# Performance work log

Measured on AMD Instinct MI355X. Metric: run time of the kernel, lower is better.

Reference implementation:

```python
import jax, jax.numpy as jnp
import numpy as np

N_NODES = 100000
N_EDGES = 3200000
F_IN, F_HID, F_OUT = 1433, 8, 7
K = 2  # kernel_size, dim=1, degree-1 B-spline -> basis (1-u, u)
LEAKY_SLOPE = 0.2


def att_spline_conv(x, edge_index, pseudo, w, root, att, bias, n_nodes):
    """Attention SplineConv layer (dim=1, kernel_size=2, linear B-spline).

    w:    [K, in, out] spline kernel weights
    root: [in, out]    root/self weight
    att:  [2*out]      attention vector (src-message part || dst part)
    """
    src, dst = edge_index[0], edge_index[1]
    u = pseudo[:, 0]                                   # [E], in [0,1]
    basis = jnp.stack([1.0 - u, u], axis=1)            # [E, K]
    # transform at node level first (cheap), then gather per edge
    xw = jnp.einsum('ni,kio->nko', x, w)               # [N, K, out]
    m = jnp.einsum('ek,eko->eo', basis, xw[src])       # [E, out] spline message
    h = x @ root                                       # [N, out] root transform
    out_dim = w.shape[-1]
    # GAT-style attention: leaky_relu(a_src . m_e + a_dst . h_dst)
    score = m @ att[:out_dim] + (h @ att[out_dim:])[dst]   # [E]
    score = jax.nn.leaky_relu(score, LEAKY_SLOPE)
    smax = jax.ops.segment_max(score, dst, num_segments=n_nodes)
    e = jnp.exp(score - smax[dst])
    denom = jax.ops.segment_sum(e, dst, num_segments=n_nodes)
    alpha = e / (denom[dst] + 1e-16)                   # segment softmax over dst
    agg = jax.ops.segment_sum(alpha[:, None] * m, dst, num_segments=n_nodes)
    return agg + h + bias


def setup_inputs() -> dict:
    key = jax.random.key(0)
    ks = jax.random.split(key, 12)
    x = jax.random.normal(ks[0], (N_NODES, F_IN), dtype=jnp.float32)
    edge_index = jax.random.randint(ks[1], (2, N_EDGES), 0, N_NODES, dtype=jnp.int64)
    pseudo = jax.random.uniform(ks[2], (N_EDGES, 1), dtype=jnp.float32)
    s1 = 1.0 / np.sqrt(F_IN)
    s2 = 1.0 / np.sqrt(F_HID)
    return {
        'x': x,
        'edge_index': edge_index,
        'pseudo': pseudo,
        'w1': jax.random.normal(ks[3], (K, F_IN, F_HID), dtype=jnp.float32) * s1,
        'root1': jax.random.normal(ks[4], (F_IN, F_HID), dtype=jnp.float32) * s1,
        'att1': jax.random.normal(ks[5], (2 * F_HID,), dtype=jnp.float32) * s2,
        'bias1': jnp.zeros((F_HID,), dtype=jnp.float32),
        'w2': jax.random.normal(ks[6], (K, F_HID, F_OUT), dtype=jnp.float32) * s2,
        'root2': jax.random.normal(ks[7], (F_HID, F_OUT), dtype=jnp.float32) * s2,
        'att2': jax.random.normal(ks[8], (2 * F_OUT,), dtype=jnp.float32) * s2,
        'bias2': jnp.zeros((F_OUT,), dtype=jnp.float32),
    }


def reference(x, edge_index, pseudo, w1, root1, att1, bias1, w2, root2, att2, bias2):
    # eval mode: F.dropout with training=False is identity
    n = x.shape[0]
    h = jax.nn.elu(att_spline_conv(x, edge_index, pseudo, w1, root1, att1, bias1, n))
    h = att_spline_conv(h, edge_index, pseudo, w2, root2, att2, bias2, n)
    return jax.nn.log_softmax(h, axis=1)
```

## Files before the change

### kernel.cpp

```cpp
#include <hip/hip_runtime.h>
#include <math.h>

#define TPB 256
#define F_IN 1433
#define KPAD 1440
#define NT 45
#define NFULL 44
#define ROWS 128

typedef __attribute__((ext_vector_type(8))) short bf16x8;
typedef __attribute__((ext_vector_type(4))) float f32x4;

static __device__ __forceinline__ short f2bf(float f) {
    unsigned u = __float_as_uint(f);
    unsigned r = (u + 0x7FFFu + ((u >> 16) & 1u)) >> 16;
    return (short)r;
}

__global__ __launch_bounds__(256) void prep_kernel(
    const float* __restrict__ w1, const float* __restrict__ root1,
    short* __restrict__ WT, int* __restrict__ cnt, int N)
{
    int i = blockIdx.x * 256 + threadIdx.x;
    if (i < N) cnt[i] = 0;
    if (i < 32 * KPAD) {
        int col = i / KPAD, k = i - col * KPAD;
        float v = 0.f;
        if (k < F_IN) {
            if (col < 8)       v = w1[(size_t)k * 8 + col];
            else if (col < 16) v = w1[(size_t)(F_IN + k) * 8 + (col - 8)];
            else if (col < 24) v = root1[(size_t)k * 8 + (col - 16)];
        }
        WT[i] = f2bf(v);
    }
}

__global__ __launch_bounds__(256) void node1_hist_kernel(
    const float* __restrict__ x,
    const short* __restrict__ WT,
    const float* __restrict__ att1,
    float* __restrict__ XW1,
    float* __restrict__ H1,
    float2* __restrict__ SC1,
    float* __restrict__ HA1,
    const int* __restrict__ ei,
    int* __restrict__ cnt,
    int N, int E, int NB1)
{
    __shared__ float xb[4][32][32];

    const int tid = threadIdx.x;
    const int bid = blockIdx.x;

    if (bid >= NB1) {
        int e = (bid - NB1) * TPB + tid;
        if (e < E) atomicAdd(&cnt[ei[(size_t)E + e]], 1);
        return;
    }

    const int wv   = tid >> 6;
    const int lane = tid & 63;
    const int rowbase = bid * ROWS;

    const int srow   = lane & 7;
    const int schunk = lane >> 3;
    const int pchunk = schunk ^ srow;
    const float* gsrc[4];
#pragma unroll
    for (int g = 0; g < 4; ++g) {
        int r = rowbase + wv * 32 + g * 8 + srow;
        if (r >= N) r = N - 1;
        gsrc[g] = x + (size_t)r * F_IN + schunk * 4;
    }

    const int r0 = lane & 15, r1 = r0 + 16;
    const int klane = (lane >> 4) * 8;
    const int c0 = klane >> 2;
    const int p0 = c0 ^ (r0 & 7);
    const int p1 = (c0 + 1) ^ (r0 & 7);
    const short* wt0 = WT + (size_t)(lane & 15) * KPAD + klane;
    const short* wt1 = wt0 + 16 * KPAD;

    f32x4 acc[2][2];
#pragma unroll
    for (int i = 0; i < 2; ++i)
#pragma unroll
        for (int j = 0; j < 2; ++j)
#pragma unroll
            for (int r = 0; r < 4; ++r) acc[i][j][r] = 0.f;

    {
        float4 V[4];
#pragma unroll
        for (int g = 0; g < 4; ++g) V[g] = *reinterpret_cast<const float4*>(gsrc[g]);
#pragma unroll
        for (int g = 0; g < 4; ++g)
            *reinterpret_cast<float4*>(&xb[wv][g * 8 + srow][pchunk * 4]) = V[g];
    }

    for (int t = 0; t < NFULL; ++t) {
        float4 Vn[4];
        const bool more = (t + 1 < NFULL);
        if (more) {
#pragma unroll
            for (int g = 0; g < 4; ++g)
                Vn[g] = *reinterpret_cast<const float4*>(gsrc[g] + (t + 1) * 32);
        }
        bf16x8 b0 = *reinterpret_cast<const bf16x8*>(wt0 + t * 32);
        bf16x8 b1 = *reinterpret_cast<const bf16x8*>(wt1 + t * 32);
        float4 fa0 = *reinterpret_cast<const float4*>(&xb[wv][r0][p0 * 4]);
        float4 fb0 = *reinterpret_cast<const float4*>(&xb[wv][r0][p1 * 4]);
        float4 fa1 = *reinterpret_cast<const float4*>(&xb[wv][r1][p0 * 4]);
        float4 fb1 = *reinterpret_cast<const float4*>(&xb[wv][r1][p1 * 4]);
        bf16x8 pa0, pa1;
        pa0[0] = f2bf(fa0.x); pa0[1] = f2bf(fa0.y); pa0[2] = f2bf(fa0.z); pa0[3] = f2bf(fa0.w);
        pa0[4] = f2bf(fb0.x); pa0[5] = f2bf(fb0.y); pa0[6] = f2bf(fb0.z); pa0[7] = f2bf(fb0.w);
        pa1[0] = f2bf(fa1.x); pa1[1] = f2bf(fa1.y); pa1[2] = f2bf(fa1.z); pa1[3] = f2bf(fa1.w);
        pa1[4] = f2bf(fb1.x); pa1[5] = f2bf(fb1.y); pa1[6] = f2bf(fb1.z); pa1[7] = f2bf(fb1.w);
        acc[0][0] = __builtin_amdgcn_mfma_f32_16x16x32_bf16(pa0, b0, acc[0][0], 0, 0, 0);
        acc[0][1] = __builtin_amdgcn_mfma_f32_16x16x32_bf16(pa0, b1, acc[0][1], 0, 0, 0);
        acc[1][0] = __builtin_amdgcn_mfma_f32_16x16x32_bf16(pa1, b0, acc[1][0], 0, 0, 0);
        acc[1][1] = __builtin_amdgcn_mfma_f32_16x16x32_bf16(pa1, b1, acc[1][1], 0, 0, 0);
        if (more) {
#pragma unroll
            for (int g = 0; g < 4; ++g)
                *reinterpret_cast<float4*>(&xb[wv][g * 8 + srow][pchunk * 4]) = Vn[g];
        }
    }

    {
        int rr0 = rowbase + wv * 32 + r0; if (rr0 >= N) rr0 = N - 1;
        int rr1 = rowbase + wv * 32 + r1; if (rr1 >= N) rr1 = N - 1;
        const float* xr0 = x + (size_t)rr0 * F_IN;
        const float* xr1 = x + (size_t)rr1 * F_IN;
        const int kf = NFULL * 32 + klane;
        bf16x8 pa0, pa1;
#pragma unroll
        for (int q = 0; q < 8; ++q) {
            float v0 = (kf + q < F_IN) ? xr0[kf + q] : 0.f;
            float v1 = (kf + q < F_IN) ? xr1[kf + q] : 0.f;
            pa0[q] = f2bf(v0);
            pa1[q] = f2bf(v1);
        }
        bf16x8 b0 = *reinterpret_cast<const bf16x8*>(wt0 + NFULL * 32);
        bf16x8 b1 = *reinterpret_cast<const bf16x8*>(wt1 + NFULL * 32);
        acc[0][0] = __builtin_amdgcn_mfma_f32_16x16x32_bf16(pa0, b0, acc[0][0], 0, 0, 0);
        acc[0][1] = __builtin_amdgcn_mfma_f32_16x16x32_bf16(pa0, b1, acc[0][1], 0, 0, 0);
        acc[1][0] = __builtin_amdgcn_mfma_f32_16x16x32_bf16(pa1, b0, acc[1][0], 0, 0, 0);
        acc[1][1] = __builtin_amdgcn_mfma_f32_16x16x32_bf16(pa1, b1, acc[1][1], 0, 0, 0);
    }

    __syncthreads();

    float* dump = reinterpret_cast<float*>(xb);
#pragma unroll
    for (int rt = 0; rt < 2; ++rt)
#pragma unroll
        for (int ot = 0; ot < 2; ++ot) {
            int col = ot * 16 + (lane & 15);
            if (col < 24) {
#pragma unroll
                for (int r = 0; r < 4; ++r) {
                    int row = wv * 32 + rt * 16 + (lane >> 4) * 4 + r;
                    dump[row * 25 + col] = acc[rt][ot][r];
                }
            }
        }
    __syncthreads();

    if (tid < ROWS) {
        int n = rowbase + tid;
        if (n < N) {
            float sum[24];
#pragma unroll
            for (int j = 0; j < 24; ++j) sum[j] = dump[tid * 25 + j];
            float s0 = 0.f, s1 = 0.f, ha = 0.f;
#pragma unroll
            for (int j = 0; j < 8; ++j) {
                s0 += sum[j] * att1[j];
                s1 += sum[8 + j] * att1[j];
                ha += sum[16 + j] * att1[8 + j];
            }
            float4* xwout = reinterpret_cast<float4*>(XW1 + (size_t)n * 16);
            xwout[0] = make_float4(sum[0], sum[1], sum[2], sum[3]);
            xwout[1] = make_float4(sum[4], sum[5], sum[6], sum[7]);
            xwout[2] = make_float4(sum[8], sum[9], sum[10], sum[11]);
            xwout[3] = make_float4(sum[12], sum[13], sum[14], sum[15]);
            float4* hout = reinterpret_cast<float4*>(H1 + (size_t)n * 8);
            hout[0] = make_float4(sum[16], sum[17], sum[18], sum[19]);
            hout[1] = make_float4(sum[20], sum[21], sum[22], sum[23]);
            SC1[n] = make_float2(s0, s1);
            HA1[n] = ha;
        }
    }
}

__global__ __launch_bounds__(256) void scanA_kernel(
    const int* __restrict__ cnt, int* __restrict__ rowptr, int* __restrict__ bsums, int N)
{
    __shared__ int lds[256];
    int t = threadIdx.x;
    int base = blockIdx.x * 1024 + t * 4;
    int c[4];
#pragma unroll
    for (int j = 0; j < 4; ++j) c[j] = (base + j < N) ? cnt[base + j] : 0;
    int tsum = c[0] + c[1] + c[2] + c[3];
    lds[t] = tsum;
    __syncthreads();
    for (int off = 1; off < 256; off <<= 1) {
        int v = (t >= off) ? lds[t - off] : 0;
        __syncthreads();
        lds[t] += v;
        __syncthreads();
    }
    int run = lds[t] - tsum;
#pragma unroll
    for (int j = 0; j < 4; ++j) {
        if (base + j < N) rowptr[base + j] = run;
        run += c[j];
    }
    if (t == 255) bsums[blockIdx.x] = lds[255];
}

__global__ __launch_bounds__(128) void scanB_kernel(int* __restrict__ bsums, int nb)
{
    __shared__ int lds[128];
    int t = threadIdx.x;
    int v = (t < nb) ? bsums[t] : 0;
    lds[t] = v;
    __syncthreads();
    for (int off = 1; off < 128; off <<= 1) {
        int w = (t >= off) ? lds[t - off] : 0;
        __syncthreads();
        lds[t] += w;
        __syncthreads();
    }
    if (t < nb) bsums[t] = lds[t] - v;
}

__global__ __launch_bounds__(256) void scanC_kernel(
    int* __restrict__ rowptr, int* __restrict__ cnt, const int* __restrict__ bsums, int N, int E)
{
    int i = blockIdx.x * TPB + threadIdx.x;
    if (i < N) {
        int v = rowptr[i] + bsums[i >> 10];
        rowptr[i] = v;
        cnt[i] = v;
    }
    if (i == 0) rowptr[N] = E;
}

__global__ __launch_bounds__(256) void scatter_kernel(
    const int* __restrict__ ei, const float* __restrict__ pseudo,
    int* __restrict__ cursor, int2* __restrict__ recs, int E)
{
    int e = blockIdx.x * TPB + threadIdx.x;
    if (e >= E) return;
    int s = ei[e];
    int d = ei[(size_t)E + e];
    float u = pseudo[e];
    int pos = atomicAdd(&cursor[d], 1);
    recs[pos] = make_int2(s, __float_as_int(u));
}

__global__ __launch_bounds__(256) void gather1_kernel(
    const int* __restrict__ rowptr, const int2* __restrict__ recs,
    const float4* __restrict__ XW1v,
    const float2* __restrict__ SC1, const float* __restrict__ HA1,
    const float* __restrict__ H1, const float* __restrict__ bias1,
    const float* __restrict__ w2, const float* __restrict__ root2, const float* __restrict__ att2,
    float* __restrict__ XW2, float* __restrict__ H2, float2* __restrict__ SC2, float* __restrict__ HA2,
    int N)
{
    int tid = blockIdx.x * TPB + threadIdx.x;
    int n = tid >> 4;
    int lane = tid & 15;
    if (n >= N) return;
    int start = rowptr[n], end = rowptr[n + 1];
    float ha = HA1[n];
    float den = 0.f;
    float num[8];
#pragma unroll
    for (int j = 0; j < 8; ++j) num[j] = 0.f;

    for (int i = start + lane; i < end; i += 16) {
        int2 r = recs[i];
        int s = r.x;
        float u = __int_as_float(r.y);
        float um = 1.f - u;
        float2 sc = SC1[s];
        float raw = um * sc.x + u * sc.y + ha;
        float score = (raw > 0.f) ? raw : 0.2f * raw;
        float w = expf(score);
        const float4* xw = XW1v + (size_t)s * 4;
        float4 p0 = xw[0], p1 = xw[1], q0 = xw[2], q1 = xw[3];
        num[0] = fmaf(w, um * p0.x + u * q0.x, num[0]);
        num[1] = fmaf(w, um * p0.y + u * q0.y, num[1]);
        num[2] = fmaf(w, um * p0.z + u * q0.z, num[2]);
        num[3] = fmaf(w, um * p0.w + u * q0.w, num[3]);
        num[4] = fmaf(w, um * p1.x + u * q1.x, num[4]);
        num[5] = fmaf(w, um * p1.y + u * q1.y, num[5]);
        num[6] = fmaf(w, um * p1.z + u * q1.z, num[6]);
        num[7] = fmaf(w, um * p1.w + u * q1.w, num[7]);
        den += w;
    }
#pragma unroll
    for (int off = 1; off < 16; off <<= 1) {
#pragma unroll
        for (int j = 0; j < 8; ++j) num[j] += __shfl_xor(num[j], off);
        den += __shfl_xor(den, off);
    }
    if (lane != 0) return;

    float inv = 1.f / (den + 1e-16f);
    float hp[8];
#pragma unroll
    for (int j = 0; j < 8; ++j) {
        float o = num[j] * inv + H1[(size_t)n * 8 + j] + bias1[j];
        hp[j] = (o > 0.f) ? o : expm1f(o);
    }
    float a[7], b[7], h[7];
#pragma unroll
    for (int j2 = 0; j2 < 7; ++j2) { a[j2] = 0.f; b[j2] = 0.f; h[j2] = 0.f; }
#pragma unroll
    for (int j = 0; j < 8; ++j) {
#pragma unroll
        for (int j2 = 0; j2 < 7; ++j2) {
            a[j2] = fmaf(hp[j], w2[j * 7 + j2], a[j2]);
            b[j2] = fmaf(hp[j], w2[56 + j * 7 + j2], b[j2]);
            h[j2] = fmaf(hp[j], root2[j * 7 + j2], h[j2]);
        }
    }
    float s0 = 0.f, s1 = 0.f, hA = 0.f;
#pragma unroll
    for (int j2 = 0; j2 < 7; ++j2) {
        s0 += a[j2] * att2[j2];
        s1 += b[j2] * att2[j2];
        hA += h[j2] * att2[7 + j2];
    }
    float4* xwout = reinterpret_cast<float4*>(XW2 + (size_t)n * 16);
    xwout[0] = make_float4(a[0], a[1], a[2], a[3]);
    xwout[1] = make_float4(a[4], a[5], a[6], 0.f);
    xwout[2] = make_float4(b[0], b[1], b[2], b[3]);
    xwout[3] = make_float4(b[4], b[5], b[6], 0.f);
    float4* hout = reinterpret_cast<float4*>(H2 + (size_t)n * 8);
    hout[0] = make_float4(h[0], h[1], h[2], h[3]);
    hout[1] = make_float4(h[4], h[5], h[6], 0.f);
    SC2[n] = make_float2(s0, s1);
    HA2[n] = hA;
}

__global__ __launch_bounds__(256) void gather2_kernel(
    const int* __restrict__ rowptr, const int2* __restrict__ recs,
    const float4* __restrict__ XW2v,
    const float2* __restrict__ SC2, const float* __restrict__ HA2,
    const float* __restrict__ H2, const float* __restrict__ bias2,
    float* __restrict__ out, int N)
{
    int tid = blockIdx.x * TPB + threadIdx.x;
    int n = tid >> 4;
    int lane = tid & 15;
    if (n >= N) return;
    int start = rowptr[n], end = rowptr[n + 1];
    float ha = HA2[n];
    float den = 0.f;
    float num[7];
#pragma unroll
    for (int j = 0; j < 7; ++j) num[j] = 0.f;

    for (int i = start + lane; i < end; i += 16) {
        int2 r = recs[i];
        int s = r.x;
        float u = __int_as_float(r.y);
        float um = 1.f - u;
        float2 sc = SC2[s];
        float raw = um * sc.x + u * sc.y + ha;
        float score = (raw > 0.f) ? raw : 0.2f * raw;
        float w = expf(score);
        const float4* xw = XW2v + (size_t)s * 4;
        float4 p0 = xw[0], p1 = xw[1], q0 = xw[2], q1 = xw[3];
        num[0] = fmaf(w, um * p0.x + u * q0.x, num[0]);
        num[1] = fmaf(w, um * p0.y + u * q0.y, num[1]);
        num[2] = fmaf(w, um * p0.z + u * q0.z, num[2]);
        num[3] = fmaf(w, um * p0.w + u * q0.w, num[3]);
        num[4] = fmaf(w, um * p1.x + u * q1.x, num[4]);
        num[5] = fmaf(w, um * p1.y + u * q1.y, num[5]);
        num[6] = fmaf(w, um * p1.z + u * q1.z, num[6]);
        den += w;
    }
#pragma unroll
    for (int off = 1; off < 16; off <<= 1) {
#pragma unroll
        for (int j = 0; j < 7; ++j) num[j] += __shfl_xor(num[j], off);
        den += __shfl_xor(den, off);
    }
    if (lane != 0) return;

    float inv = 1.f / (den + 1e-16f);
    float o[7];
    float mx = -1e30f;
#pragma unroll
    for (int j = 0; j < 7; ++j) {
        o[j] = fmaf(num[j], inv, H2[(size_t)n * 8 + j] + bias2[j]);
        mx = fmaxf(mx, o[j]);
    }
    float sum = 0.f;
#pragma unroll
    for (int j = 0; j < 7; ++j) sum += expf(o[j] - mx);
    float lse = mx + logf(sum);
#pragma unroll
    for (int j = 0; j < 7; ++j) out[(size_t)n * 7 + j] = o[j] - lse;
}

extern "C" void kernel_launch(void* const* d_in, const int* in_sizes, int n_in,
                              void* d_out, int out_size, void* d_ws, size_t ws_size,
                              hipStream_t stream) {
    const float* x      = (const float*)d_in[0];
    const int*   ei     = (const int*)d_in[1];
    const float* pseudo = (const float*)d_in[2];
    const float* w1     = (const float*)d_in[3];
    const float* root1  = (const float*)d_in[4];
    const float* att1   = (const float*)d_in[5];
    const float* bias1  = (const float*)d_in[6];
    const float* w2     = (const float*)d_in[7];
    const float* root2  = (const float*)d_in[8];
    const float* att2   = (const float*)d_in[9];
    const float* bias2  = (const float*)d_in[10];

    const int N = in_sizes[0] / F_IN;
    const int E = in_sizes[2];
    const size_t Ns = (size_t)N;

    float* ws   = (float*)d_ws;
    float* XW1  = ws;
    float* H1   = XW1 + 16 * Ns;
    float2* SC1 = (float2*)(H1 + 8 * Ns);
    float* HA1  = (float*)SC1 + 2 * Ns;
    float* XW2  = HA1 + Ns;
    float* H2   = XW2 + 16 * Ns;
    float2* SC2 = (float2*)(H2 + 8 * Ns);
    float* HA2  = (float*)SC2 + 2 * Ns;
    int*   cnt    = (int*)(HA2 + Ns);
    int*   rowptr = cnt + Ns;
    int*   bsums  = rowptr + Ns + 1;
    size_t off = (size_t)(bsums + 128) - (size_t)d_ws;
    off = (off + 7) & ~(size_t)7;
    int2*  recs = (int2*)((char*)d_ws + off);
    size_t woff = off + (size_t)E * sizeof(int2);
    woff = (woff + 15) & ~(size_t)15;
    short* WT = (short*)((char*)d_ws + woff);

    int nblk  = (N + TPB - 1) / TPB;
    int eblk  = (E + TPB - 1) / TPB;
    int sblkA = (N + 1023) / 1024;
    int nb1   = (N + ROWS - 1) / ROWS;
    int gblk  = ((N * 16) + TPB - 1) / TPB;
    int prepn = (32 * KPAD > N) ? 32 * KPAD : N;
    int pblk  = (prepn + TPB - 1) / TPB;

    prep_kernel<<<pblk, TPB, 0, stream>>>(w1, root1, WT, cnt, N);
    node1_hist_kernel<<<nb1 + eblk, TPB, 0, stream>>>(
        x, WT, att1, XW1, H1, SC1, HA1, ei, cnt, N, E, nb1);
    scanA_kernel<<<sblkA, TPB, 0, stream>>>(cnt, rowptr, bsums, N);
    scanB_kernel<<<1, 128, 0, stream>>>(bsums, sblkA);
    scanC_kernel<<<nblk, TPB, 0, stream>>>(rowptr, cnt, bsums, N, E);
    scatter_kernel<<<eblk, TPB, 0, stream>>>(ei, pseudo, cnt, recs, E);
    gather1_kernel<<<gblk, TPB, 0, stream>>>(rowptr, recs, (const float4*)XW1, SC1, HA1,
                                             H1, bias1, w2, root2, att2,
                                             XW2, H2, SC2, HA2, N);
    gather2_kernel<<<gblk, TPB, 0, stream>>>(rowptr, recs, (const float4*)XW2, SC2, HA2,
                                             H2, bias2, (float*)d_out, N);
}
```

Before: 611.1 us.

## Load x directly into MFMA operands with 4-deep register prefetch, drop LDS staging

The first-layer node GEMM no longer stages x tiles through swizzled shared memory. Each lane now loads its own fp32 x row segment straight into registers, with a four-stage register prefetch pipeline. Each wave handles 16 rows instead of 32, so the block covers 64 rows and there are twice as many blocks. The gather kernels also switch expf and logf to the fast __expf and __logf intrinsics. This removes LDS traffic and gives more memory parallelism, at the cost of less coalesced per-lane global loads (each lane reads 32 contiguous bytes per row) and slightly lower precision in the exponentials.

```diff
diff --git a/kernel.cpp b/kernel.cpp
--- a/kernel.cpp
+++ b/kernel.cpp
@@ -6,7 +6,7 @@
 #define KPAD 1440
 #define NT 45
 #define NFULL 44
-#define ROWS 128
+#define BROWS 64
 
 typedef __attribute__((ext_vector_type(8))) short bf16x8;
 typedef __attribute__((ext_vector_type(4))) float f32x4;
@@ -47,7 +47,7 @@
     int* __restrict__ cnt,
     int N, int E, int NB1)
 {
-    __shared__ float xb[4][32][32];
+    __shared__ float dump[BROWS * 25];
 
     const int tid = threadIdx.x;
     const int bid = blockIdx.x;
@@ -60,115 +60,88 @@
 
     const int wv   = tid >> 6;
     const int lane = tid & 63;
-    const int rowbase = bid * ROWS;
-
-    const int srow   = lane & 7;
-    const int schunk = lane >> 3;
-    const int pchunk = schunk ^ srow;
-    const float* gsrc[4];
-#pragma unroll
-    for (int g = 0; g < 4; ++g) {
-        int r = rowbase + wv * 32 + g * 8 + srow;
-        if (r >= N) r = N - 1;
-        gsrc[g] = x + (size_t)r * F_IN + schunk * 4;
-    }
-
-    const int r0 = lane & 15, r1 = r0 + 16;
-    const int klane = (lane >> 4) * 8;
-    const int c0 = klane >> 2;
-    const int p0 = c0 ^ (r0 & 7);
-    const int p1 = (c0 + 1) ^ (r0 & 7);
-    const short* wt0 = WT + (size_t)(lane & 15) * KPAD + klane;
+    const int rowbase = bid * BROWS;
+
+    const int r0 = lane & 15;
+    const int kg = lane >> 4;
+    const int klane = kg * 8;
+    int rr = rowbase + wv * 16 + r0;
+    if (rr >= N) rr = N - 1;
+    const float* xr = x + (size_t)rr * F_IN;
+    const short* wt0 = WT + (size_t)r0 * KPAD + klane;
     const short* wt1 = wt0 + 16 * KPAD;
 
-    f32x4 acc[2][2];
-#pragma unroll
-    for (int i = 0; i < 2; ++i)
-#pragma unroll
-        for (int j = 0; j < 2; ++j)
-#pragma unroll
-            for (int r = 0; r < 4; ++r) acc[i][j][r] = 0.f;
+    f32x4 acc0, acc1;
+#pragma unroll
+    for (int r = 0; r < 4; ++r) { acc0[r] = 0.f; acc1[r] = 0.f; }
+
+#define LOADT(t, Aa, Ab, Ba, Bb) do {                                          \
+        const float* p_ = xr + (t) * 32 + klane;                               \
+        Aa = *reinterpret_cast<const float4*>(p_);                             \
+        Ab = *reinterpret_cast<const float4*>(p_ + 4);                         \
+        Ba = *reinterpret_cast<const bf16x8*>(wt0 + (t) * 32);                 \
+        Bb = *reinterpret_cast<const bf16x8*>(wt1 + (t) * 32);                 \
+    } while (0)
+
+#define COMP(Aa, Ab, Ba, Bb) do {                                              \
+        bf16x8 pa_;                                                            \
+        pa_[0] = f2bf(Aa.x); pa_[1] = f2bf(Aa.y);                              \
+        pa_[2] = f2bf(Aa.z); pa_[3] = f2bf(Aa.w);                              \
+        pa_[4] = f2bf(Ab.x); pa_[5] = f2bf(Ab.y);                              \
+        pa_[6] = f2bf(Ab.z); pa_[7] = f2bf(Ab.w);                              \
+        acc0 = __builtin_amdgcn_mfma_f32_16x16x32_bf16(pa_, Ba, acc0, 0, 0, 0);\
+        acc1 = __builtin_amdgcn_mfma_f32_16x16x32_bf16(pa_, Bb, acc1, 0, 0, 0);\
+    } while (0)
+
+    float4 A00, A01, A10, A11, A20, A21, A30, A31;
+    bf16x8 B00, B01, B10, B11, B20, B21, B30, B31;
+
+    LOADT(0, A00, A01, B00, B01);
+    LOADT(1, A10, A11, B10, B11);
+    LOADT(2, A20, A21, B20, B21);
+    LOADT(3, A30, A31, B30, B31);
+
+    for (int t = 0; t < NFULL; t += 4) {
+        COMP(A00, A01, B00, B01);
+        if (t + 4 < NFULL) LOADT(t + 4, A00, A01, B00, B01);
+        COMP(A10, A11, B10, B11);
+        if (t + 5 < NFULL) LOADT(t + 5, A10, A11, B10, B11);
+        COMP(A20, A21, B20, B21);
+        if (t + 6 < NFULL) LOADT(t + 6, A20, A21, B20, B21);
+        COMP(A30, A31, B30, B31);
+        if (t + 7 < NFULL) LOADT(t + 7, A30, A31, B30, B31);
+    }
+#undef LOADT
+#undef COMP
 
     {
-        float4 V[4];
-#pragma unroll
-        for (int g = 0; g < 4; ++g) V[g] = *reinterpret_cast<const float4*>(gsrc[g]);
-#pragma unroll
-        for (int g = 0; g < 4; ++g)
-            *reinterpret_cast<float4*>(&xb[wv][g * 8 + srow][pchunk * 4]) = V[g];
-    }
-
-    for (int t = 0; t < NFULL; ++t) {
-        float4 Vn[4];
-        const bool more = (t + 1 < NFULL);
-        if (more) {
-#pragma unroll
-            for (int g = 0; g < 4; ++g)
-                Vn[g] = *reinterpret_cast<const float4*>(gsrc[g] + (t + 1) * 32);
-        }
-        bf16x8 b0 = *reinterpret_cast<const bf16x8*>(wt0 + t * 32);
-        bf16x8 b1 = *reinterpret_cast<const bf16x8*>(wt1 + t * 32);
-        float4 fa0 = *reinterpret_cast<const float4*>(&xb[wv][r0][p0 * 4]);
-        float4 fb0 = *reinterpret_cast<const float4*>(&xb[wv][r0][p1 * 4]);
-        float4 fa1 = *reinterpret_cast<const float4*>(&xb[wv][r1][p0 * 4]);
-        float4 fb1 = *reinterpret_cast<const float4*>(&xb[wv][r1][p1 * 4]);
-        bf16x8 pa0, pa1;
-        pa0[0] = f2bf(fa0.x); pa0[1] = f2bf(fa0.y); pa0[2] = f2bf(fa0.z); pa0[3] = f2bf(fa0.w);
-        pa0[4] = f2bf(fb0.x); pa0[5] = f2bf(fb0.y); pa0[6] = f2bf(fb0.z); pa0[7] = f2bf(fb0.w);
-        pa1[0] = f2bf(fa1.x); pa1[1] = f2bf(fa1.y); pa1[2] = f2bf(fa1.z); pa1[3] = f2bf(fa1.w);
-        pa1[4] = f2bf(fb1.x); pa1[5] = f2bf(fb1.y); pa1[6] = f2bf(fb1.z); pa1[7] = f2bf(fb1.w);
-        acc[0][0] = __builtin_amdgcn_mfma_f32_16x16x32_bf16(pa0, b0, acc[0][0], 0, 0, 0);
-        acc[0][1] = __builtin_amdgcn_mfma_f32_16x16x32_bf16(pa0, b1, acc[0][1], 0, 0, 0);
-        acc[1][0] = __builtin_amdgcn_mfma_f32_16x16x32_bf16(pa1, b0, acc[1][0], 0, 0, 0);
-        acc[1][1] = __builtin_amdgcn_mfma_f32_16x16x32_bf16(pa1, b1, acc[1][1], 0, 0, 0);
-        if (more) {
-#pragma unroll
-            for (int g = 0; g < 4; ++g)
-                *reinterpret_cast<float4*>(&xb[wv][g * 8 + srow][pchunk * 4]) = Vn[g];
-        }
-    }
-
-    {
-        int rr0 = rowbase + wv * 32 + r0; if (rr0 >= N) rr0 = N - 1;
-        int rr1 = rowbase + wv * 32 + r1; if (rr1 >= N) rr1 = N - 1;
-        const float* xr0 = x + (size_t)rr0 * F_IN;
-        const float* xr1 = x + (size_t)rr1 * F_IN;
         const int kf = NFULL * 32 + klane;
-        bf16x8 pa0, pa1;
+        bf16x8 pa;
 #pragma unroll
         for (int q = 0; q < 8; ++q) {
-            float v0 = (kf + q < F_IN) ? xr0[kf + q] : 0.f;
-            float v1 = (kf + q < F_IN) ? xr1[kf + q] : 0.f;
-            pa0[q] = f2bf(v0);
-            pa1[q] = f2bf(v1);
+            float v = (kf + q < F_IN) ? xr[kf + q] : 0.f;
+            pa[q] = f2bf(v);
         }
         bf16x8 b0 = *reinterpret_cast<const bf16x8*>(wt0 + NFULL * 32);
         bf16x8 b1 = *reinterpret_cast<const bf16x8*>(wt1 + NFULL * 32);
-        acc[0][0] = __builtin_amdgcn_mfma_f32_16x16x32_bf16(pa0, b0, acc[0][0], 0, 0, 0);
-        acc[0][1] = __builtin_amdgcn_mfma_f32_16x16x32_bf16(pa0, b1, acc[0][1], 0, 0, 0);
-        acc[1][0] = __builtin_amdgcn_mfma_f32_16x16x32_bf16(pa1, b0, acc[1][0], 0, 0, 0);
-        acc[1][1] = __builtin_amdgcn_mfma_f32_16x16x32_bf16(pa1, b1, acc[1][1], 0, 0, 0);
-    }
-
-    __syncthreads();
-
-    float* dump = reinterpret_cast<float*>(xb);
-#pragma unroll
-    for (int rt = 0; rt < 2; ++rt)
-#pragma unroll
-        for (int ot = 0; ot < 2; ++ot) {
-            int col = ot * 16 + (lane & 15);
-            if (col < 24) {
-#pragma unroll
-                for (int r = 0; r < 4; ++r) {
-                    int row = wv * 32 + rt * 16 + (lane >> 4) * 4 + r;
-                    dump[row * 25 + col] = acc[rt][ot][r];
-                }
+        acc0 = __builtin_amdgcn_mfma_f32_16x16x32_bf16(pa, b0, acc0, 0, 0, 0);
+        acc1 = __builtin_amdgcn_mfma_f32_16x16x32_bf16(pa, b1, acc1, 0, 0, 0);
+    }
+
+#pragma unroll
+    for (int ot = 0; ot < 2; ++ot) {
+        int col = ot * 16 + (lane & 15);
+        if (col < 24) {
+#pragma unroll
+            for (int r = 0; r < 4; ++r) {
+                int row = wv * 16 + kg * 4 + r;
+                dump[row * 25 + col] = (ot == 0) ? acc0[r] : acc1[r];
             }
         }
+    }
     __syncthreads();
 
-    if (tid < ROWS) {
+    if (tid < BROWS) {
         int n = rowbase + tid;
         if (n < N) {
             float sum[24];
@@ -291,7 +264,7 @@
         float2 sc = SC1[s];
         float raw = um * sc.x + u * sc.y + ha;
         float score = (raw > 0.f) ? raw : 0.2f * raw;
-        float w = expf(score);
+        float w = __expf(score);
         const float4* xw = XW1v + (size_t)s * 4;
         float4 p0 = xw[0], p1 = xw[1], q0 = xw[2], q1 = xw[3];
         num[0] = fmaf(w, um * p0.x + u * q0.x, num[0]);
@@ -376,7 +349,7 @@
         float2 sc = SC2[s];
         float raw = um * sc.x + u * sc.y + ha;
         float score = (raw > 0.f) ? raw : 0.2f * raw;
-        float w = expf(score);
+        float w = __expf(score);
         const float4* xw = XW2v + (size_t)s * 4;
         float4 p0 = xw[0], p1 = xw[1], q0 = xw[2], q1 = xw[3];
         num[0] = fmaf(w, um * p0.x + u * q0.x, num[0]);
@@ -406,8 +379,8 @@
     }
     float sum = 0.f;
 #pragma unroll
-    for (int j = 0; j < 7; ++j) sum += expf(o[j] - mx);
-    float lse = mx + logf(sum);
+    for (int j = 0; j < 7; ++j) sum += __expf(o[j] - mx);
+    float lse = mx + __logf(sum);
 #pragma unroll
     for (int j = 0; j < 7; ++j) out[(size_t)n * 7 + j] = o[j] - lse;
 }
@@ -453,7 +426,7 @@
     int nblk  = (N + TPB - 1) / TPB;
     int eblk  = (E + TPB - 1) / TPB;
     int sblkA = (N + 1023) / 1024;
-    int nb1   = (N + ROWS - 1) / ROWS;
+    int nb1   = (N + BROWS - 1) / BROWS;
     int gblk  = ((N * 16) + TPB - 1) / TPB;
     int prepn = (32 * KPAD > N) ? 32 * KPAD : N;
     int pblk  = (prepn + TPB - 1) / TPB;
```

Result: slower. 645.9 us (+5.7%).

## Split histogram out of node GEMM kernel, vectorize it, use fast exp/log

Applied to the files above, without the earlier changes.

Separates the edge-degree histogram from the node-level MFMA transform into its own kernel launched afterwards. The histogram now processes four edges per thread with an int4 load. Per-edge attention exponentials and the final log-softmax switch to __expf/__logf intrinsics. This gives up the overlap of the atomic histogram with the GEMM and adds a launch, in exchange for fewer threads and fewer loads in the histogram and cheaper transcendentals.

```diff
diff --git a/kernel.cpp b/kernel.cpp
--- a/kernel.cpp
+++ b/kernel.cpp
@@ -35,7 +35,23 @@
     }
 }
 
-__global__ __launch_bounds__(256) void node1_hist_kernel(
+__global__ __launch_bounds__(256) void hist_kernel(
+    const int* __restrict__ ei, int* __restrict__ cnt, int E)
+{
+    int t = blockIdx.x * TPB + threadIdx.x;
+    int base = t * 4;
+    if (base + 4 <= E) {
+        int4 d = *reinterpret_cast<const int4*>(ei + (size_t)E + base);
+        atomicAdd(&cnt[d.x], 1);
+        atomicAdd(&cnt[d.y], 1);
+        atomicAdd(&cnt[d.z], 1);
+        atomicAdd(&cnt[d.w], 1);
+    } else {
+        for (int e = base; e < E; ++e) atomicAdd(&cnt[ei[(size_t)E + e]], 1);
+    }
+}
+
+__global__ __launch_bounds__(256) void node1_kernel(
     const float* __restrict__ x,
     const short* __restrict__ WT,
     const float* __restrict__ att1,
@@ -43,20 +59,12 @@
     float* __restrict__ H1,
     float2* __restrict__ SC1,
     float* __restrict__ HA1,
-    const int* __restrict__ ei,
-    int* __restrict__ cnt,
-    int N, int E, int NB1)
+    int N)
 {
     __shared__ float xb[4][32][32];
 
     const int tid = threadIdx.x;
     const int bid = blockIdx.x;
-
-    if (bid >= NB1) {
-        int e = (bid - NB1) * TPB + tid;
-        if (e < E) atomicAdd(&cnt[ei[(size_t)E + e]], 1);
-        return;
-    }
 
     const int wv   = tid >> 6;
     const int lane = tid & 63;
@@ -78,7 +86,7 @@
     const int c0 = klane >> 2;
     const int p0 = c0 ^ (r0 & 7);
     const int p1 = (c0 + 1) ^ (r0 & 7);
-    const short* wt0 = WT + (size_t)(lane & 15) * KPAD + klane;
+    const short* wt0 = WT + (size_t)(lane & 15) * KPAD;
     const short* wt1 = wt0 + 16 * KPAD;
 
     f32x4 acc[2][2];
@@ -106,8 +114,8 @@
             for (int g = 0; g < 4; ++g)
                 Vn[g] = *reinterpret_cast<const float4*>(gsrc[g] + (t + 1) * 32);
         }
-        bf16x8 b0 = *reinterpret_cast<const bf16x8*>(wt0 + t * 32);
-        bf16x8 b1 = *reinterpret_cast<const bf16x8*>(wt1 + t * 32);
+        bf16x8 b0 = *reinterpret_cast<const bf16x8*>(wt0 + t * 32 + klane);
+        bf16x8 b1 = *reinterpret_cast<const bf16x8*>(wt1 + t * 32 + klane);
         float4 fa0 = *reinterpret_cast<const float4*>(&xb[wv][r0][p0 * 4]);
         float4 fb0 = *reinterpret_cast<const float4*>(&xb[wv][r0][p1 * 4]);
         float4 fa1 = *reinterpret_cast<const float4*>(&xb[wv][r1][p0 * 4]);
@@ -142,8 +150,8 @@
             pa0[q] = f2bf(v0);
             pa1[q] = f2bf(v1);
         }
-        bf16x8 b0 = *reinterpret_cast<const bf16x8*>(wt0 + NFULL * 32);
-        bf16x8 b1 = *reinterpret_cast<const bf16x8*>(wt1 + NFULL * 32);
+        bf16x8 b0 = *reinterpret_cast<const bf16x8*>(wt0 + NFULL * 32 + klane);
+        bf16x8 b1 = *reinterpret_cast<const bf16x8*>(wt1 + NFULL * 32 + klane);
         acc[0][0] = __builtin_amdgcn_mfma_f32_16x16x32_bf16(pa0, b0, acc[0][0], 0, 0, 0);
         acc[0][1] = __builtin_amdgcn_mfma_f32_16x16x32_bf16(pa0, b1, acc[0][1], 0, 0, 0);
         acc[1][0] = __builtin_amdgcn_mfma_f32_16x16x32_bf16(pa1, b0, acc[1][0], 0, 0, 0);
@@ -291,7 +299,7 @@
         float2 sc = SC1[s];
         float raw = um * sc.x + u * sc.y + ha;
         float score = (raw > 0.f) ? raw : 0.2f * raw;
-        float w = expf(score);
+        float w = __expf(score);
         const float4* xw = XW1v + (size_t)s * 4;
         float4 p0 = xw[0], p1 = xw[1], q0 = xw[2], q1 = xw[3];
         num[0] = fmaf(w, um * p0.x + u * q0.x, num[0]);
@@ -376,7 +384,7 @@
         float2 sc = SC2[s];
         float raw = um * sc.x + u * sc.y + ha;
         float score = (raw > 0.f) ? raw : 0.2f * raw;
-        float w = expf(score);
+        float w = __expf(score);
         const float4* xw = XW2v + (size_t)s * 4;
         float4 p0 = xw[0], p1 = xw[1], q0 = xw[2], q1 = xw[3];
         num[0] = fmaf(w, um * p0.x + u * q0.x, num[0]);
@@ -406,8 +414,8 @@
     }
     float sum = 0.f;
 #pragma unroll
-    for (int j = 0; j < 7; ++j) sum += expf(o[j] - mx);
-    float lse = mx + logf(sum);
+    for (int j = 0; j < 7; ++j) sum += __expf(o[j] - mx);
+    float lse = mx + __logf(sum);
 #pragma unroll
     for (int j = 0; j < 7; ++j) out[(size_t)n * 7 + j] = o[j] - lse;
 }
@@ -452,6 +460,7 @@
 
     int nblk  = (N + TPB - 1) / TPB;
     int eblk  = (E + TPB - 1) / TPB;
+    int hblk  = (E / 4 + TPB - 1) / TPB;
     int sblkA = (N + 1023) / 1024;
     int nb1   = (N + ROWS - 1) / ROWS;
     int gblk  = ((N * 16) + TPB - 1) / TPB;
@@ -459,8 +468,9 @@
     int pblk  = (prepn + TPB - 1) / TPB;
 
     prep_kernel<<<pblk, TPB, 0, stream>>>(w1, root1, WT, cnt, N);
-    node1_hist_kernel<<<nb1 + eblk, TPB, 0, stream>>>(
-        x, WT, att1, XW1, H1, SC1, HA1, ei, cnt, N, E, nb1);
+    node1_kernel<<<nb1, TPB, 0, stream>>>(
+        x, WT, att1, XW1, H1, SC1, HA1, N);
+    hist_kernel<<<hblk, TPB, 0, stream>>>(ei, cnt, E);
     scanA_kernel<<<sblkA, TPB, 0, stream>>>(cnt, rowptr, bsums, N);
     scanB_kernel<<<1, 128, 0, stream>>>(bsums, sblkA);
     scanC_kernel<<<nblk, TPB, 0, stream>>>(rowptr, cnt, bsums, N, E);
```

Measured after the change: 693.4 us. 1.13x slower.
